# Kernel optimization log

Measured on AMD Instinct MI355X. Metric: run time of the kernel, lower is better.

Reference implementation:

```python
import jax, jax.numpy as jnp
import numpy as np

B, L, DIM, H, D = 4, 1024, 1024, 8, 32


def setup_inputs() -> dict:
    key = jax.random.key(0)
    ks = jax.random.split(key, 8)
    s = 0.02
    return dict(
        x=jax.random.normal(ks[0], (B, L, DIM), jnp.float32),
        W_in=jax.random.normal(ks[1], (DIM, DIM), jnp.float32) * s,
        b_in=jnp.zeros((DIM,), jnp.float32),
        W_qkva=jax.random.normal(ks[2], (H * D * 8, DIM), jnp.float32) * s,
        b_qkva=jnp.zeros((H * D * 8,), jnp.float32),
        W_y=jax.random.normal(ks[3], (DIM, H * D * 2), jnp.float32) * s,
        b_y=jnp.zeros((DIM,), jnp.float32),
        W_out=jax.random.normal(ks[4], (DIM, DIM), jnp.float32) * s,
        b_out=jnp.zeros((DIM,), jnp.float32),
        h0_re=jax.random.normal(ks[5], (H, D, D), jnp.float32),
        h0_im=jax.random.normal(ks[6], (H, D, D), jnp.float32),
    )


def reference(x, W_in, b_in, W_qkva, b_qkva, W_y, b_y, W_out, b_out, h0_re, h0_im):
    b, Ls, dim = x.shape
    Hh, Dd = h0_re.shape[0], h0_re.shape[1]
    u = jax.nn.silu(x @ W_in.T + b_in)
    qkva = (u @ W_qkva.T + b_qkva).reshape(b, Ls, Hh, Dd, 4, 2)
    c = jax.lax.complex(qkva[..., 0], qkva[..., 1])  # [b,L,H,D,4] complex
    q, k, v, a = c[..., 0], c[..., 1], c[..., 2], c[..., 3]
    mag2 = a.real * a.real + a.imag * a.imag
    # unit-modulus rotation scaled by sigmoid(log|a|^2) gate
    a = a * (jax.lax.rsqrt(mag2) * jax.nn.sigmoid(jnp.log(mag2)))
    kv = jnp.einsum('blhd,blhe->blhde', k, v)  # [b,L,H,D,D] complex
    h0 = jax.lax.complex(h0_re, h0_im)[None]  # [1,H,D,D]
    # fold initial state into step 0: h_0 = a_0 * h_init + kv_0
    kv = kv.at[:, 0].add(a[:, 0, ..., None] * h0)
    a_e = a[..., None]  # [b,L,H,D,1], broadcasts over state col dim

    def comb(c1, c2):
        a1, x1 = c1
        a2, x2 = c2
        return (a1 * a2, a2 * x1 + x2)

    # linear recurrence h_l = a_l * h_{l-1} + kv_l (equiv. to the FFT/cumsum
    # triangular-product matrix in the original module)
    _, h = jax.lax.associative_scan(comb, (a_e, kv), axis=1)
    y = jnp.einsum('blhd,blhde->blhe', q, h)  # [b,L,H,D] complex
    y2 = jnp.stack([y.real, y.imag], axis=-1).reshape(b, Ls, Hh * Dd * 2)
    y2 = jax.nn.silu(y2 @ W_y.T + b_y)
    return y2 @ W_out.T + b_out
```

## Files before the change

### kernel.cpp

```cpp
#include <hip/hip_runtime.h>

#define B_ 4
#define L_ 1024
#define DIM_ 1024
#define H_ 8
#define D_ 32
#define LSEG 16
#define NSEG (L_/LSEG)

typedef __bf16 bf16_t;
typedef __bf16 bf16x8 __attribute__((ext_vector_type(8)));
typedef float f32x4 __attribute__((ext_vector_type(4)));

__device__ __forceinline__ void gload_lds16(const bf16_t* g, bf16_t* l) {
  __builtin_amdgcn_global_load_lds((const __attribute__((address_space(1))) void*)g,
                                   (__attribute__((address_space(3))) void*)l, 16, 0, 0);
}
__device__ __forceinline__ void gload_lds16f(const float* g, float* l) {
  __builtin_amdgcn_global_load_lds((const __attribute__((address_space(1))) void*)g,
                                   (__attribute__((address_space(3))) void*)l, 16, 0, 0);
}

__global__ __launch_bounds__(256) void cvt_all(const float* __restrict__ x,
                                               const float* __restrict__ w1,
                                               const float* __restrict__ w2,
                                               const float* __restrict__ w3,
                                               const float* __restrict__ w4,
                                               bf16_t* __restrict__ ox,
                                               bf16_t* __restrict__ o1,
                                               bf16_t* __restrict__ o2,
                                               bf16_t* __restrict__ o3,
                                               bf16_t* __restrict__ o4) {
  int g = blockIdx.x;
  const float* in; bf16_t* out; int i;
  if      (g < 4096) { in = x;  out = ox; i = g * 256 + threadIdx.x; }
  else if (g < 5120) { in = w1; out = o1; i = (g - 4096) * 256 + threadIdx.x; }
  else if (g < 7168) { in = w2; out = o2; i = (g - 5120) * 256 + threadIdx.x; }
  else if (g < 7680) { in = w3; out = o3; i = (g - 7168) * 256 + threadIdx.x; }
  else               { in = w4; out = o4; i = (g - 7680) * 256 + threadIdx.x; }
  float4 v = ((const float4*)in)[i];
  union { bf16_t b[4]; unsigned long long q; } pk;
  pk.b[0] = (bf16_t)v.x; pk.b[1] = (bf16_t)v.y;
  pk.b[2] = (bf16_t)v.z; pk.b[3] = (bf16_t)v.w;
  ((unsigned long long*)out)[i] = pk.q;
}

template<int BN, int ACT, int OUTBF, int GATE>
__global__ __launch_bounds__(256) void gemm_nt(const bf16_t* __restrict__ A,
                                               const bf16_t* __restrict__ Bm,
                                               const float* __restrict__ bias,
                                               void* __restrict__ Cout,
                                               int M, int N, int K) {
  constexpr int NI = BN / 32;
  constexpr int ISS_B = BN / 32;
  __shared__ __align__(16) bf16_t As[128 * 64];
  __shared__ __align__(16) bf16_t Bs[BN * 64];
  const int t = threadIdx.x;
  const int wid = t >> 6, lane = t & 63;
  const int wr = wid >> 1, wc = wid & 1;
  const int lr = lane & 15, lq = lane >> 4;
  const int bm = blockIdx.x, bn = blockIdx.y;
  const int rA = wid * 32 + (lane >> 3);
  const int rB = wid * (BN / 4) + (lane >> 3);
  const int c8 = (((lane & 7) ^ ((lane >> 3) & 7))) * 8;
  const bf16_t* Ag = A + (size_t)(bm * 128 + rA) * K + c8;
  const bf16_t* Bg = Bm + (size_t)(bn * BN + rB) * K + c8;
  bf16_t* AsW = As + (wid * 32) * 64;
  bf16_t* BsW = Bs + (wid * (BN / 4)) * 64;
  f32x4 acc[4][NI] = {};
  for (int k0 = 0; k0 < K; k0 += 64) {
#pragma unroll
    for (int j = 0; j < 4; ++j)
      gload_lds16(Ag + (size_t)j * 8 * K, AsW + j * 8 * 64);
#pragma unroll
    for (int j = 0; j < ISS_B; ++j)
      gload_lds16(Bg + (size_t)j * 8 * K, BsW + j * 8 * 64);
    Ag += 64; Bg += 64;
    __syncthreads();
#pragma unroll
    for (int ks = 0; ks < 2; ++ks) {
      const int sg = ks * 4 + lq;
      const int sl = (sg ^ (lr & 7)) * 8;
      bf16x8 af[4], bfv[NI];
#pragma unroll
      for (int mi = 0; mi < 4; ++mi)
        af[mi] = *(const bf16x8*)&As[(wr * 64 + mi * 16 + lr) * 64 + sl];
#pragma unroll
      for (int ni = 0; ni < NI; ++ni)
        bfv[ni] = *(const bf16x8*)&Bs[(wc * (BN/2) + ni * 16 + lr) * 64 + sl];
#pragma unroll
      for (int mi = 0; mi < 4; ++mi)
#pragma unroll
        for (int ni = 0; ni < NI; ++ni)
          acc[mi][ni] = __builtin_amdgcn_mfma_f32_16x16x32_bf16(af[mi], bfv[ni], acc[mi][ni], 0, 0, 0);
    }
    __syncthreads();
  }
#pragma unroll
  for (int mi = 0; mi < 4; ++mi) {
#pragma unroll
    for (int ni = 0; ni < NI; ++ni) {
      int colg = bn * BN + wc * (BN/2) + ni * 16 + lr;
      float bb = bias[colg];
#pragma unroll
      for (int r = 0; r < 4; ++r) {
        int rowg = bm * 128 + wr * 64 + mi * 16 + lq * 4 + r;
        float v = acc[mi][ni][r] + bb;
        if (ACT == 1) v = v / (1.0f + __expf(-v));
        if (GATE) {
          float wv = __shfl_xor(v, 1);
          if ((colg & 7) >= 6) {
            float m2 = v * v + wv * wv;
            v *= sqrtf(m2) / (1.0f + m2);
          }
        }
        if (OUTBF) ((bf16_t*)Cout)[(size_t)rowg * N + colg] = (bf16_t)v;
        else       ((float*)Cout)[(size_t)rowg * N + colg] = v;
      }
    }
  }
}

template<int ACT, int OUTBF>
__global__ __launch_bounds__(256) void gemm_nt64(const bf16_t* __restrict__ A,
                                                 const bf16_t* __restrict__ Bm,
                                                 const float* __restrict__ bias,
                                                 void* __restrict__ Cout,
                                                 int M, int N, int K) {
  __shared__ __align__(16) bf16_t As[128 * 128];
  __shared__ __align__(16) bf16_t Bs[64 * 128];
  const int t = threadIdx.x;
  const int wid = t >> 6, lane = t & 63;
  const int wr = wid >> 1, wc = wid & 1;
  const int lr = lane & 15, lq = lane >> 4;
  const int bm = blockIdx.x, bn = blockIdx.y;
  const int crow = wid * 4 + (lane >> 4);
  const int c8 = ((lane & 15) ^ crow) * 8;
  const bf16_t* Ag = A + (size_t)(bm * 128 + crow) * K + c8;
  const bf16_t* Bg = Bm + (size_t)(bn * 64 + crow) * K + c8;
  bf16_t* AsW = As + (wid * 4) * 128;
  bf16_t* BsW = Bs + (wid * 4) * 128;
  f32x4 acc[4][2] = {};
  for (int k0 = 0; k0 < K; k0 += 128) {
#pragma unroll
    for (int j = 0; j < 8; ++j)
      gload_lds16(Ag + (size_t)j * 16 * K, AsW + j * 16 * 128);
#pragma unroll
    for (int j = 0; j < 4; ++j)
      gload_lds16(Bg + (size_t)j * 16 * K, BsW + j * 16 * 128);
    Ag += 128; Bg += 128;
    __syncthreads();
#pragma unroll
    for (int ks = 0; ks < 4; ++ks) {
      const int sg = ks * 4 + lq;
      const int sl = (sg ^ lr) * 8;
      bf16x8 af[4], bfv[2];
#pragma unroll
      for (int mi = 0; mi < 4; ++mi)
        af[mi] = *(const bf16x8*)&As[(wr * 64 + mi * 16 + lr) * 128 + sl];
#pragma unroll
      for (int ni = 0; ni < 2; ++ni)
        bfv[ni] = *(const bf16x8*)&Bs[(wc * 32 + ni * 16 + lr) * 128 + sl];
#pragma unroll
      for (int mi = 0; mi < 4; ++mi)
#pragma unroll
        for (int ni = 0; ni < 2; ++ni)
          acc[mi][ni] = __builtin_amdgcn_mfma_f32_16x16x32_bf16(af[mi], bfv[ni], acc[mi][ni], 0, 0, 0);
    }
    __syncthreads();
  }
#pragma unroll
  for (int mi = 0; mi < 4; ++mi) {
#pragma unroll
    for (int ni = 0; ni < 2; ++ni) {
      int colg = bn * 64 + wc * 32 + ni * 16 + lr;
      float bb = bias[colg];
#pragma unroll
      for (int r = 0; r < 4; ++r) {
        int rowg = bm * 128 + wr * 64 + mi * 16 + lq * 4 + r;
        float v = acc[mi][ni][r] + bb;
        if (ACT == 1) v = v / (1.0f + __expf(-v));
        if (OUTBF) ((bf16_t*)Cout)[(size_t)rowg * N + colg] = (bf16_t)v;
        else       ((float*)Cout)[(size_t)rowg * N + colg] = v;
      }
    }
  }
}

__global__ __launch_bounds__(256) void scan_seg(const float* __restrict__ qkva,
                                                float* __restrict__ y_loc,
                                                float* __restrict__ qP,
                                                float* __restrict__ Aseg,
                                                float* __restrict__ Hfin) {
  __shared__ __align__(16) float Q[LSEG * 256];
  const int t = threadIdx.x;
  const int seg = blockIdx.x;
  const int s = seg & (NSEG - 1);
  const int bh = seg >> 6;
  const int h = bh & (H_ - 1), b = bh >> 3;
  const int wid = t >> 6, lane = t & 63;
  const int dg = lane & 7, eh = lane >> 3;
  const int e = wid * 8 + eh;
  const float* gb = qkva + ((size_t)(b * L_ + s * LSEG) * H_ + h) * 256;
#pragma unroll
  for (int j = 0; j < 4; ++j) {
    const int l = wid * 4 + j;
    gload_lds16f(gb + (size_t)l * (H_ * 256) + lane * 4, Q + l * 256);
  }
  __syncthreads();
  float hr[4] = {}, hi[4] = {};
  float Pr[4] = {1,1,1,1}, Pi[4] = {0,0,0,0};
  size_t row = ((size_t)(b * L_ + s * LSEG) * H_ + h) * D_;
  for (int l = 0; l < LSEG; ++l) {
    const float* R = Q + l * 256;
    float2 vv = *(const float2*)(R + e * 8 + 4);
    float ytr = 0.f, yti = 0.f;
    float2 qpv[4];
#pragma unroll
    for (int j = 0; j < 4; ++j) {
      const int d = dg + 8 * j;
      float4 qk = *(const float4*)(R + d * 8);
      float2 aa = *(const float2*)(R + d * 8 + 6);
      float nPr = aa.x * Pr[j] - aa.y * Pi[j];
      float nPi = aa.x * Pi[j] + aa.y * Pr[j];
      Pr[j] = nPr; Pi[j] = nPi;
      qpv[j].x = qk.x * nPr - qk.y * nPi;
      qpv[j].y = qk.x * nPi + qk.y * nPr;
      float kvr = qk.z * vv.x - qk.w * vv.y;
      float kvi = qk.z * vv.y + qk.w * vv.x;
      float nhr = aa.x * hr[j] - aa.y * hi[j] + kvr;
      float nhi = aa.x * hi[j] + aa.y * hr[j] + kvi;
      hr[j] = nhr; hi[j] = nhi;
      ytr += qk.x * nhr - qk.y * nhi;
      yti += qk.x * nhi + qk.y * nhr;
    }
    ytr += __shfl_down(ytr, 4); yti += __shfl_down(yti, 4);
    ytr += __shfl_down(ytr, 2); yti += __shfl_down(yti, 2);
    ytr += __shfl_down(ytr, 1); yti += __shfl_down(yti, 1);
    if (dg == 0)
      *(float2*)(y_loc + (row + e) * 2) = make_float2(ytr, yti);
    if (t < 8) {
#pragma unroll
      for (int j = 0; j < 4; ++j)
        *(float2*)(qP + (row + dg + 8 * j) * 2) = qpv[j];
    }
    row += H_ * D_;
  }
  const size_t segb = (size_t)seg * D_;
  if (t < 8) {
#pragma unroll
    for (int j = 0; j < 4; ++j)
      *(float2*)(Aseg + (segb + dg + 8 * j) * 2) = make_float2(Pr[j], Pi[j]);
  }
#pragma unroll
  for (int j = 0; j < 4; ++j)
    *(float2*)(Hfin + ((segb + dg + 8 * j) * D_ + e) * 2) = make_float2(hr[j], hi[j]);
}

__global__ __launch_bounds__(128) void seg_combine(const float* __restrict__ h0re,
                                                   const float* __restrict__ h0im,
                                                   const float* __restrict__ Aseg,
                                                   const float* __restrict__ Hfin,
                                                   float* __restrict__ Hc) {
  const int bh = blockIdx.x >> 3;
  const int eg = blockIdx.x & 7;
  const int h = bh & (H_ - 1);
  const int t = threadIdx.x;
  const int d = t >> 2;
  const int e = eg * 4 + (t & 3);
  float cr = h0re[((size_t)h * D_ + d) * D_ + e];
  float ci = h0im[((size_t)h * D_ + d) * D_ + e];
  const size_t idx0  = ((size_t)bh * NSEG * D_ + d) * D_ + e;
  const size_t aidx0 = (size_t)bh * NSEG * D_ + d;
  float2 Ab[8], Fb[8];
#pragma unroll
  for (int p = 0; p < 8; ++p) {
    Ab[p] = *(const float2*)(Aseg + (aidx0 + (size_t)p * D_) * 2);
    Fb[p] = *(const float2*)(Hfin + (idx0 + (size_t)p * D_ * D_) * 2);
  }
  for (int so = 0; so < NSEG; so += 8) {
#pragma unroll
    for (int p = 0; p < 8; ++p) {
      const int s = so + p;
      float2 A0 = Ab[p], F0 = Fb[p];
      if (so + 8 < NSEG) {
        Ab[p] = *(const float2*)(Aseg + (aidx0 + (size_t)(s + 8) * D_) * 2);
        Fb[p] = *(const float2*)(Hfin + (idx0 + (size_t)(s + 8) * D_ * D_) * 2);
      }
      *(float2*)(Hc + (idx0 + (size_t)s * D_ * D_) * 2) = make_float2(cr, ci);
      float nr = A0.x * cr - A0.y * ci + F0.x;
      float ni = A0.x * ci + A0.y * cr + F0.y;
      cr = nr; ci = ni;
    }
  }
}

__global__ __launch_bounds__(256) void y_correct(const float* __restrict__ y_loc,
                                                 const float* __restrict__ qP,
                                                 const float* __restrict__ Hc,
                                                 bf16_t* __restrict__ y2b) {
  __shared__ __align__(16) float Hs[D_ * D_ * 2];
  const int seg = blockIdx.x;
  const int s = seg & (NSEG - 1);
  const int bh = seg >> 6;
  const int h = bh & (H_ - 1), b = bh >> 3;
  const int t = threadIdx.x;
  const float4* src = (const float4*)(Hc + (size_t)seg * (D_ * D_ * 2));
  ((float4*)Hs)[t] = src[t];
  ((float4*)Hs)[t + 256] = src[t + 256];
  __syncthreads();
  const int l = t >> 4;
  const int ep = (t & 15) * 2;
  const int lg = s * LSEG + l;
  const size_t rowc = ((size_t)(b * L_ + lg) * H_ + h) * D_;
  const float* qpr = qP + rowc * 2;
  float4 y0 = *(const float4*)(y_loc + (rowc + ep) * 2);
  float ac_r[2] = {y0.x, y0.z}, ac_i[2] = {y0.y, y0.w};
#pragma unroll 4
  for (int d = 0; d < D_; ++d) {
    float2 p = *(const float2*)(qpr + d * 2);
    float4 hv = *(const float4*)&Hs[(d * D_ + ep) * 2];
    ac_r[0] += p.x * hv.x - p.y * hv.y; ac_i[0] += p.x * hv.y + p.y * hv.x;
    ac_r[1] += p.x * hv.z - p.y * hv.w; ac_i[1] += p.x * hv.w + p.y * hv.z;
  }
  union { bf16_t bv[4]; uint2 q; } pk;
  pk.bv[0] = (bf16_t)ac_r[0]; pk.bv[1] = (bf16_t)ac_i[0];
  pk.bv[2] = (bf16_t)ac_r[1]; pk.bv[3] = (bf16_t)ac_i[1];
  *(uint2*)(y2b + (size_t)(b * L_ + lg) * (H_ * D_ * 2) + (h * D_ + ep) * 2) = pk.q;
}

extern "C" void kernel_launch(void* const* d_in, const int* in_sizes, int n_in,
                              void* d_out, int out_size, void* d_ws, size_t ws_size,
                              hipStream_t stream) {
  const float* x      = (const float*)d_in[0];
  const float* W_in   = (const float*)d_in[1];
  const float* b_in   = (const float*)d_in[2];
  const float* W_qkva = (const float*)d_in[3];
  const float* b_qkva = (const float*)d_in[4];
  const float* W_y    = (const float*)d_in[5];
  const float* b_y    = (const float*)d_in[6];
  const float* W_out  = (const float*)d_in[7];
  const float* b_out  = (const float*)d_in[8];
  const float* h0re   = (const float*)d_in[9];
  const float* h0im   = (const float*)d_in[10];

  char* w = (char*)d_ws;
  const size_t MB = 1ull << 20;
  bf16_t* Wb_in   = (bf16_t*)(w + 0*MB);
  bf16_t* Wb_qkva = (bf16_t*)(w + 2*MB);
  bf16_t* Wb_y    = (bf16_t*)(w + 6*MB);
  bf16_t* Wb_out  = (bf16_t*)(w + 7*MB);
  bf16_t* xb      = (bf16_t*)(w + 9*MB);
  float*  qP      = (float*) (w + 9*MB);
  bf16_t* u       = (bf16_t*)(w + 17*MB);
  float*  y_loc   = (float*) (w + 17*MB);
  float*  qkva    = (float*) (w + 25*MB);
  float*  Hc      = (float*) (w + 25*MB);
  bf16_t* y2b     = (bf16_t*)(w + 41*MB);
  bf16_t* z       = (bf16_t*)(w + 45*MB);
  float*  Aseg    = (float*) (w + 57*MB);
  float*  Hfin    = (float*) (w + 58*MB);

  cvt_all<<<8704, 256, 0, stream>>>(x, W_in, W_qkva, W_y, W_out,
                                    xb, Wb_in, Wb_qkva, Wb_y, Wb_out);

  gemm_nt64<1,1><<<dim3(32, 16), 256, 0, stream>>>(xb, Wb_in, b_in, u, 4096, 1024, 1024);
  gemm_nt<128,0,0,1><<<dim3(32, 16), 256, 0, stream>>>(u, Wb_qkva, b_qkva, qkva, 4096, 2048, 1024);
  scan_seg   <<<2048, 256, 0, stream>>>(qkva, y_loc, qP, Aseg, Hfin);
  seg_combine<<<256,  128, 0, stream>>>(h0re, h0im, Aseg, Hfin, Hc);
  y_correct  <<<2048, 256, 0, stream>>>(y_loc, qP, Hc, y2b);
  gemm_nt64<1,1><<<dim3(32, 16), 256, 0, stream>>>(y2b, Wb_y, b_y, z, 4096, 1024, 512);
  gemm_nt64<0,0><<<dim3(32, 16), 256, 0, stream>>>(z, Wb_out, b_out, (float*)d_out, 4096, 1024, 1024);
}
```

Baseline: 229.2 us.

## Fuse segmented scan, combine and correction into one cooperative kernel

Replaces the three-kernel chunked scan (local scan, cross-segment combine, y correction) with a single cooperative-groups kernel that uses grid-wide syncs between phases. Segments grow from 16 to 32 steps, and q·P and local y stay in shared memory instead of round-tripping through global buffers. This removes two launches and the y_loc/qP traffic. In exchange it adds grid sync overhead, a serial combine phase run by only 256 blocks, and it depends on all 1024 blocks being co-resident, with a fallback to the old path otherwise.

```diff
diff --git a/kernel.cpp b/kernel.cpp
--- a/kernel.cpp
+++ b/kernel.cpp
@@ -1,4 +1,5 @@
 #include <hip/hip_runtime.h>
+#include <hip/hip_cooperative_groups.h>
 
 #define B_ 4
 #define L_ 1024
@@ -7,6 +8,8 @@
 #define D_ 32
 #define LSEG 16
 #define NSEG (L_/LSEG)
+#define LSEG2 32
+#define NSEG2 (L_/LSEG2)
 
 typedef __bf16 bf16_t;
 typedef __bf16 bf16x8 __attribute__((ext_vector_type(8)));
@@ -184,6 +187,159 @@
         else       ((float*)Cout)[(size_t)rowg * N + colg] = v;
       }
     }
+  }
+}
+
+__global__ __launch_bounds__(256, 4) void scan_fused(
+    const float* qkva,
+    const float* __restrict__ h0re,
+    const float* __restrict__ h0im,
+    float* __restrict__ Aseg,
+    float* __restrict__ Hfin,
+    float* Hc,
+    bf16_t* y2b) {
+  __shared__ __align__(16) float S[LSEG2 * 256];
+  const int t = threadIdx.x;
+  const int seg = blockIdx.x;
+  const int s = seg & (NSEG2 - 1);
+  const int bh = seg >> 5;
+  const int h = bh & (H_ - 1), b = bh >> 3;
+  const int wid = t >> 6, lane = t & 63;
+  const int dg = lane & 7, eh = lane >> 3;
+  const int e = wid * 8 + eh;
+
+  const float* gb = qkva + ((size_t)(b * L_ + s * LSEG2) * H_ + h) * 256;
+#pragma unroll
+  for (int j = 0; j < 8; ++j) {
+    const int l = wid * 8 + j;
+    gload_lds16f(gb + (size_t)l * (H_ * 256) + lane * 4, S + l * 256);
+  }
+  __syncthreads();
+  float hr[4] = {}, hi[4] = {};
+  float Pr[4] = {1,1,1,1}, Pi[4] = {0,0,0,0};
+  for (int l = 0; l < LSEG2; ++l) {
+    const float* R = S + l * 256;
+    float2 vv = *(const float2*)(R + e * 8 + 4);
+    float ytr = 0.f, yti = 0.f;
+    float2 qpv[4];
+#pragma unroll
+    for (int j = 0; j < 4; ++j) {
+      const int d = dg + 8 * j;
+      float4 qk = *(const float4*)(R + d * 8);
+      float2 aa = *(const float2*)(R + d * 8 + 6);
+      float nPr = aa.x * Pr[j] - aa.y * Pi[j];
+      float nPi = aa.x * Pi[j] + aa.y * Pr[j];
+      Pr[j] = nPr; Pi[j] = nPi;
+      qpv[j].x = qk.x * nPr - qk.y * nPi;
+      qpv[j].y = qk.x * nPi + qk.y * nPr;
+      float kvr = qk.z * vv.x - qk.w * vv.y;
+      float kvi = qk.z * vv.y + qk.w * vv.x;
+      float nhr = aa.x * hr[j] - aa.y * hi[j] + kvr;
+      float nhi = aa.x * hi[j] + aa.y * hr[j] + kvi;
+      hr[j] = nhr; hi[j] = nhi;
+      ytr += qk.x * nhr - qk.y * nhi;
+      yti += qk.x * nhi + qk.y * nhr;
+    }
+    ytr += __shfl_down(ytr, 4); yti += __shfl_down(yti, 4);
+    ytr += __shfl_down(ytr, 2); yti += __shfl_down(yti, 2);
+    ytr += __shfl_down(ytr, 1); yti += __shfl_down(yti, 1);
+    __syncthreads();
+    if (t < 8) {
+#pragma unroll
+      for (int j = 0; j < 4; ++j) {
+        const int d = dg + 8 * j;
+        *(float2*)(S + l * 256 + ((d + l * 4) & 31) * 2) = qpv[j];
+      }
+    }
+    if (dg == 0)
+      *(float2*)(S + l * 256 + 64 + ((e + l * 4) & 31) * 2) = make_float2(ytr, yti);
+  }
+  const size_t segb = (size_t)seg * D_;
+  if (t < 8) {
+#pragma unroll
+    for (int j = 0; j < 4; ++j)
+      *(float2*)(Aseg + (segb + dg + 8 * j) * 2) = make_float2(Pr[j], Pi[j]);
+  }
+#pragma unroll
+  for (int j = 0; j < 4; ++j)
+    *(float2*)(Hfin + ((segb + dg + 8 * j) * D_ + e) * 2) = make_float2(hr[j], hi[j]);
+
+  cooperative_groups::this_grid().sync();
+
+  if (seg < 256 && t < 128) {
+    const int bh2 = seg >> 3;
+    const int eg = seg & 7;
+    const int h2 = bh2 & (H_ - 1);
+    const int d2 = t >> 2;
+    const int e2 = eg * 4 + (t & 3);
+    float cr = h0re[((size_t)h2 * D_ + d2) * D_ + e2];
+    float ci = h0im[((size_t)h2 * D_ + d2) * D_ + e2];
+    const size_t idx0  = ((size_t)bh2 * NSEG2 * D_ + d2) * D_ + e2;
+    const size_t aidx0 = (size_t)bh2 * NSEG2 * D_ + d2;
+    float2 Ab[8], Fb[8];
+#pragma unroll
+    for (int p = 0; p < 8; ++p) {
+      Ab[p] = *(const float2*)(Aseg + (aidx0 + (size_t)p * D_) * 2);
+      Fb[p] = *(const float2*)(Hfin + (idx0 + (size_t)p * D_ * D_) * 2);
+    }
+    for (int so = 0; so < NSEG2; so += 8) {
+#pragma unroll
+      for (int p = 0; p < 8; ++p) {
+        const int s2 = so + p;
+        float2 A0 = Ab[p], F0 = Fb[p];
+        if (so + 8 < NSEG2) {
+          Ab[p] = *(const float2*)(Aseg + (aidx0 + (size_t)(s2 + 8) * D_) * 2);
+          Fb[p] = *(const float2*)(Hfin + (idx0 + (size_t)(s2 + 8) * D_ * D_) * 2);
+        }
+        *(float2*)(Hc + (idx0 + (size_t)s2 * D_ * D_) * 2) = make_float2(cr, ci);
+        float nr = A0.x * cr - A0.y * ci + F0.x;
+        float ni = A0.x * ci + A0.y * cr + F0.y;
+        cr = nr; ci = ni;
+      }
+    }
+  }
+
+  cooperative_groups::this_grid().sync();
+
+  {
+    const float4* src = (const float4*)(Hc + (size_t)seg * (D_ * D_ * 2));
+#pragma unroll
+    for (int k = 0; k < 2; ++k) {
+      float4 v4 = src[k * 256 + t];
+      int F = (k * 256 + t) * 4;
+      int rw = F >> 6, j = F & 63;
+      *(float4*)(S + rw * 256 + 128 + j) = v4;
+    }
+  }
+  __syncthreads();
+  {
+    const int l = t >> 3;
+    const int tg = t & 7;
+    const int e0 = tg * 4;
+    float acr[4], aci[4];
+#pragma unroll
+    for (int i = 0; i < 4; ++i) {
+      float2 y0 = *(const float2*)(S + l * 256 + 64 + ((e0 + i + l * 4) & 31) * 2);
+      acr[i] = y0.x; aci[i] = y0.y;
+    }
+#pragma unroll 4
+    for (int d = 0; d < D_; ++d) {
+      float2 p = *(const float2*)(S + l * 256 + ((d + l * 4) & 31) * 2);
+      float4 h0v = *(const float4*)(S + d * 256 + 128 + e0 * 2);
+      float4 h1v = *(const float4*)(S + d * 256 + 128 + e0 * 2 + 4);
+      acr[0] += p.x * h0v.x - p.y * h0v.y; aci[0] += p.x * h0v.y + p.y * h0v.x;
+      acr[1] += p.x * h0v.z - p.y * h0v.w; aci[1] += p.x * h0v.w + p.y * h0v.z;
+      acr[2] += p.x * h1v.x - p.y * h1v.y; aci[2] += p.x * h1v.y + p.y * h1v.x;
+      acr[3] += p.x * h1v.z - p.y * h1v.w; aci[3] += p.x * h1v.w + p.y * h1v.z;
+    }
+    const int lg = s * LSEG2 + l;
+    union { bf16_t bv[8]; uint4 q; } pk;
+#pragma unroll
+    for (int i = 0; i < 4; ++i) {
+      pk.bv[2 * i]     = (bf16_t)acr[i];
+      pk.bv[2 * i + 1] = (bf16_t)aci[i];
+    }
+    *(uint4*)(y2b + (size_t)(b * L_ + lg) * (H_ * D_ * 2) + ((size_t)h * D_ + e0) * 2) = pk.q;
   }
 }
 
@@ -361,14 +517,31 @@
   float*  Aseg    = (float*) (w + 57*MB);
   float*  Hfin    = (float*) (w + 58*MB);
 
+  static int coop_ok = -1;
+  if (coop_ok < 0) {
+    int nb = 0;
+    hipError_t err = hipOccupancyMaxActiveBlocksPerMultiprocessor(&nb, scan_fused, 256, 0);
+    coop_ok = (err == hipSuccess && nb >= 4) ? 1 : 0;
+  }
+
   cvt_all<<<8704, 256, 0, stream>>>(x, W_in, W_qkva, W_y, W_out,
                                     xb, Wb_in, Wb_qkva, Wb_y, Wb_out);
 
   gemm_nt64<1,1><<<dim3(32, 16), 256, 0, stream>>>(xb, Wb_in, b_in, u, 4096, 1024, 1024);
   gemm_nt<128,0,0,1><<<dim3(32, 16), 256, 0, stream>>>(u, Wb_qkva, b_qkva, qkva, 4096, 2048, 1024);
-  scan_seg   <<<2048, 256, 0, stream>>>(qkva, y_loc, qP, Aseg, Hfin);
-  seg_combine<<<256,  128, 0, stream>>>(h0re, h0im, Aseg, Hfin, Hc);
-  y_correct  <<<2048, 256, 0, stream>>>(y_loc, qP, Hc, y2b);
+
+  if (coop_ok) {
+    const float* qkva_c = qkva;
+    void* args[] = { (void*)&qkva_c, (void*)&h0re, (void*)&h0im,
+                     (void*)&Aseg, (void*)&Hfin, (void*)&Hc, (void*)&y2b };
+    hipLaunchCooperativeKernel((const void*)scan_fused, dim3(1024), dim3(256),
+                               args, 0, stream);
+  } else {
+    scan_seg   <<<2048, 256, 0, stream>>>(qkva, y_loc, qP, Aseg, Hfin);
+    seg_combine<<<256,  128, 0, stream>>>(h0re, h0im, Aseg, Hfin, Hc);
+    y_correct  <<<2048, 256, 0, stream>>>(y_loc, qP, Hc, y2b);
+  }
+
   gemm_nt64<1,1><<<dim3(32, 16), 256, 0, stream>>>(y2b, Wb_y, b_y, z, 4096, 1024, 512);
   gemm_nt64<0,0><<<dim3(32, 16), 256, 0, stream>>>(z, Wb_out, b_out, (float*)d_out, 4096, 1024, 1024);
 }
```

Measured after the change: 229.9 us. No clear change (+0.3%).

## Double-buffer GEMM LDS tiles with async global-to-LDS prefetch

Applied to the files above, without the earlier changes.

Replaces the single-buffered GEMM kernels with a double-buffered variant that issues the next K-tile's global-to-LDS loads before computing on the current tile. Partial vmcnt waits and raw s_barrier calls replace full __syncthreads. The 128-wide-K gemm_nt64 kernel is dropped in favour of the 64-K double-buffered kernel at BN=64 for the three 1024-wide GEMMs. The aim is to hide global memory latency behind MFMA work, at the cost of doubled LDS use (lower occupancy) and fragile hand-counted vmcnt values.

```diff
diff --git a/kernel.cpp b/kernel.cpp
--- a/kernel.cpp
+++ b/kernel.cpp
@@ -46,15 +46,15 @@
 }
 
 template<int BN, int ACT, int OUTBF, int GATE>
-__global__ __launch_bounds__(256) void gemm_nt(const bf16_t* __restrict__ A,
+__global__ __launch_bounds__(256) void gemm_db(const bf16_t* __restrict__ A,
                                                const bf16_t* __restrict__ Bm,
                                                const float* __restrict__ bias,
                                                void* __restrict__ Cout,
                                                int M, int N, int K) {
   constexpr int NI = BN / 32;
-  constexpr int ISS_B = BN / 32;
-  __shared__ __align__(16) bf16_t As[128 * 64];
-  __shared__ __align__(16) bf16_t Bs[BN * 64];
+  constexpr int JB = BN / 32;
+  __shared__ __align__(16) bf16_t As[2][128 * 64];
+  __shared__ __align__(16) bf16_t Bs[2][BN * 64];
   const int t = threadIdx.x;
   const int wid = t >> 6, lane = t & 63;
   const int wr = wid >> 1, wc = wid & 1;
@@ -65,18 +65,32 @@
   const int c8 = (((lane & 7) ^ ((lane >> 3) & 7))) * 8;
   const bf16_t* Ag = A + (size_t)(bm * 128 + rA) * K + c8;
   const bf16_t* Bg = Bm + (size_t)(bn * BN + rB) * K + c8;
-  bf16_t* AsW = As + (wid * 32) * 64;
-  bf16_t* BsW = Bs + (wid * (BN / 4)) * 64;
   f32x4 acc[4][NI] = {};
-  for (int k0 = 0; k0 < K; k0 += 64) {
+
+  auto stage = [&](int bufi, int koff) {
+    bf16_t* AsW = &As[bufi][(wid * 32) * 64];
+    bf16_t* BsW = &Bs[bufi][(wid * (BN / 4)) * 64];
 #pragma unroll
     for (int j = 0; j < 4; ++j)
-      gload_lds16(Ag + (size_t)j * 8 * K, AsW + j * 8 * 64);
-#pragma unroll
-    for (int j = 0; j < ISS_B; ++j)
-      gload_lds16(Bg + (size_t)j * 8 * K, BsW + j * 8 * 64);
-    Ag += 64; Bg += 64;
-    __syncthreads();
+      gload_lds16(Ag + (size_t)koff + (size_t)j * 8 * K, AsW + j * 8 * 64);
+#pragma unroll
+    for (int j = 0; j < JB; ++j)
+      gload_lds16(Bg + (size_t)koff + (size_t)j * 8 * K, BsW + j * 8 * 64);
+  };
+
+  const int NT = K >> 6;
+  stage(0, 0);
+  for (int tt = 0; tt < NT; ++tt) {
+    const int cur = tt & 1;
+    if (tt + 1 < NT) {
+      stage(cur ^ 1, (tt + 1) * 64);
+      if (BN == 128) asm volatile("s_waitcnt vmcnt(8)" ::: "memory");
+      else           asm volatile("s_waitcnt vmcnt(6)" ::: "memory");
+    } else {
+      asm volatile("s_waitcnt vmcnt(0)" ::: "memory");
+    }
+    __builtin_amdgcn_s_barrier();
+    __builtin_amdgcn_sched_barrier(0);
 #pragma unroll
     for (int ks = 0; ks < 2; ++ks) {
       const int sg = ks * 4 + lq;
@@ -84,23 +98,24 @@
       bf16x8 af[4], bfv[NI];
 #pragma unroll
       for (int mi = 0; mi < 4; ++mi)
-        af[mi] = *(const bf16x8*)&As[(wr * 64 + mi * 16 + lr) * 64 + sl];
+        af[mi] = *(const bf16x8*)&As[cur][(wr * 64 + mi * 16 + lr) * 64 + sl];
 #pragma unroll
       for (int ni = 0; ni < NI; ++ni)
-        bfv[ni] = *(const bf16x8*)&Bs[(wc * (BN/2) + ni * 16 + lr) * 64 + sl];
+        bfv[ni] = *(const bf16x8*)&Bs[cur][(wc * (BN / 2) + ni * 16 + lr) * 64 + sl];
 #pragma unroll
       for (int mi = 0; mi < 4; ++mi)
 #pragma unroll
         for (int ni = 0; ni < NI; ++ni)
           acc[mi][ni] = __builtin_amdgcn_mfma_f32_16x16x32_bf16(af[mi], bfv[ni], acc[mi][ni], 0, 0, 0);
     }
-    __syncthreads();
+    __builtin_amdgcn_sched_barrier(0);
+    __builtin_amdgcn_s_barrier();
   }
 #pragma unroll
   for (int mi = 0; mi < 4; ++mi) {
 #pragma unroll
     for (int ni = 0; ni < NI; ++ni) {
-      int colg = bn * BN + wc * (BN/2) + ni * 16 + lr;
+      int colg = bn * BN + wc * (BN / 2) + ni * 16 + lr;
       float bb = bias[colg];
 #pragma unroll
       for (int r = 0; r < 4; ++r) {
@@ -114,72 +129,6 @@
             v *= sqrtf(m2) / (1.0f + m2);
           }
         }
-        if (OUTBF) ((bf16_t*)Cout)[(size_t)rowg * N + colg] = (bf16_t)v;
-        else       ((float*)Cout)[(size_t)rowg * N + colg] = v;
-      }
-    }
-  }
-}
-
-template<int ACT, int OUTBF>
-__global__ __launch_bounds__(256) void gemm_nt64(const bf16_t* __restrict__ A,
-                                                 const bf16_t* __restrict__ Bm,
-                                                 const float* __restrict__ bias,
-                                                 void* __restrict__ Cout,
-                                                 int M, int N, int K) {
-  __shared__ __align__(16) bf16_t As[128 * 128];
-  __shared__ __align__(16) bf16_t Bs[64 * 128];
-  const int t = threadIdx.x;
-  const int wid = t >> 6, lane = t & 63;
-  const int wr = wid >> 1, wc = wid & 1;
-  const int lr = lane & 15, lq = lane >> 4;
-  const int bm = blockIdx.x, bn = blockIdx.y;
-  const int crow = wid * 4 + (lane >> 4);
-  const int c8 = ((lane & 15) ^ crow) * 8;
-  const bf16_t* Ag = A + (size_t)(bm * 128 + crow) * K + c8;
-  const bf16_t* Bg = Bm + (size_t)(bn * 64 + crow) * K + c8;
-  bf16_t* AsW = As + (wid * 4) * 128;
-  bf16_t* BsW = Bs + (wid * 4) * 128;
-  f32x4 acc[4][2] = {};
-  for (int k0 = 0; k0 < K; k0 += 128) {
-#pragma unroll
-    for (int j = 0; j < 8; ++j)
-      gload_lds16(Ag + (size_t)j * 16 * K, AsW + j * 16 * 128);
-#pragma unroll
-    for (int j = 0; j < 4; ++j)
-      gload_lds16(Bg + (size_t)j * 16 * K, BsW + j * 16 * 128);
-    Ag += 128; Bg += 128;
-    __syncthreads();
-#pragma unroll
-    for (int ks = 0; ks < 4; ++ks) {
-      const int sg = ks * 4 + lq;
-      const int sl = (sg ^ lr) * 8;
-      bf16x8 af[4], bfv[2];
-#pragma unroll
-      for (int mi = 0; mi < 4; ++mi)
-        af[mi] = *(const bf16x8*)&As[(wr * 64 + mi * 16 + lr) * 128 + sl];
-#pragma unroll
-      for (int ni = 0; ni < 2; ++ni)
-        bfv[ni] = *(const bf16x8*)&Bs[(wc * 32 + ni * 16 + lr) * 128 + sl];
-#pragma unroll
-      for (int mi = 0; mi < 4; ++mi)
-#pragma unroll
-        for (int ni = 0; ni < 2; ++ni)
-          acc[mi][ni] = __builtin_amdgcn_mfma_f32_16x16x32_bf16(af[mi], bfv[ni], acc[mi][ni], 0, 0, 0);
-    }
-    __syncthreads();
-  }
-#pragma unroll
-  for (int mi = 0; mi < 4; ++mi) {
-#pragma unroll
-    for (int ni = 0; ni < 2; ++ni) {
-      int colg = bn * 64 + wc * 32 + ni * 16 + lr;
-      float bb = bias[colg];
-#pragma unroll
-      for (int r = 0; r < 4; ++r) {
-        int rowg = bm * 128 + wr * 64 + mi * 16 + lq * 4 + r;
-        float v = acc[mi][ni][r] + bb;
-        if (ACT == 1) v = v / (1.0f + __expf(-v));
         if (OUTBF) ((bf16_t*)Cout)[(size_t)rowg * N + colg] = (bf16_t)v;
         else       ((float*)Cout)[(size_t)rowg * N + colg] = v;
       }
@@ -364,11 +313,11 @@
   cvt_all<<<8704, 256, 0, stream>>>(x, W_in, W_qkva, W_y, W_out,
                                     xb, Wb_in, Wb_qkva, Wb_y, Wb_out);
 
-  gemm_nt64<1,1><<<dim3(32, 16), 256, 0, stream>>>(xb, Wb_in, b_in, u, 4096, 1024, 1024);
-  gemm_nt<128,0,0,1><<<dim3(32, 16), 256, 0, stream>>>(u, Wb_qkva, b_qkva, qkva, 4096, 2048, 1024);
+  gemm_db<64,1,1,0><<<dim3(32, 16), 256, 0, stream>>>(xb, Wb_in, b_in, u, 4096, 1024, 1024);
+  gemm_db<128,0,0,1><<<dim3(32, 16), 256, 0, stream>>>(u, Wb_qkva, b_qkva, qkva, 4096, 2048, 1024);
   scan_seg   <<<2048, 256, 0, stream>>>(qkva, y_loc, qP, Aseg, Hfin);
   seg_combine<<<256,  128, 0, stream>>>(h0re, h0im, Aseg, Hfin, Hc);
   y_correct  <<<2048, 256, 0, stream>>>(y_loc, qP, Hc, y2b);
-  gemm_nt64<1,1><<<dim3(32, 16), 256, 0, stream>>>(y2b, Wb_y, b_y, z, 4096, 1024, 512);
-  gemm_nt64<0,0><<<dim3(32, 16), 256, 0, stream>>>(z, Wb_out, b_out, (float*)d_out, 4096, 1024, 1024);
-}
+  gemm_db<64,1,1,0><<<dim3(32, 16), 256, 0, stream>>>(y2b, Wb_y, b_y, z, 4096, 1024, 512);
+  gemm_db<64,0,0,0><<<dim3(32, 16), 256, 0, stream>>>(z, Wb_out, b_out, (float*)d_out, 4096, 1024, 1024);
+}
```

Measured after the change: 232.8 us. Within noise of the previous version (+1.6%).

## Fuse x fp32-to-bf16 conversion into first GEMM and remap blocks across XCDs

Applied to the files above, without the earlier changes.

Drops the separate conversion of the 16MB fp32 input x to bf16. The first GEMM now reads fp32 x directly, converts it in registers and writes bf16 into LDS, which removes a full write and re-read of the activation through global memory. The weight-only conversion kernel stays. Separately, all GEMMs remap block IDs so consecutive tiles land on the same XCD, aiming for better L2 reuse. The fused A load goes through registers instead of direct-to-LDS loads and reads twice the bytes per tile, which may expose more load latency.

```diff
diff --git a/kernel.cpp b/kernel.cpp
--- a/kernel.cpp
+++ b/kernel.cpp
@@ -21,23 +21,28 @@
                                    (__attribute__((address_space(3))) void*)l, 16, 0, 0);
 }
 
-__global__ __launch_bounds__(256) void cvt_all(const float* __restrict__ x,
-                                               const float* __restrict__ w1,
-                                               const float* __restrict__ w2,
-                                               const float* __restrict__ w3,
-                                               const float* __restrict__ w4,
-                                               bf16_t* __restrict__ ox,
-                                               bf16_t* __restrict__ o1,
-                                               bf16_t* __restrict__ o2,
-                                               bf16_t* __restrict__ o3,
-                                               bf16_t* __restrict__ o4) {
+__device__ __forceinline__ void xcd_remap(int& bm, int& bn) {
+  const int id = blockIdx.x + 32 * blockIdx.y;
+  const int nwg = 32 * gridDim.y;
+  const int wk = (id & 7) * (nwg >> 3) + (id >> 3);
+  bm = wk & 31;
+  bn = wk >> 5;
+}
+
+__global__ __launch_bounds__(256) void cvt_w(const float* __restrict__ w1,
+                                             const float* __restrict__ w2,
+                                             const float* __restrict__ w3,
+                                             const float* __restrict__ w4,
+                                             bf16_t* __restrict__ o1,
+                                             bf16_t* __restrict__ o2,
+                                             bf16_t* __restrict__ o3,
+                                             bf16_t* __restrict__ o4) {
   int g = blockIdx.x;
   const float* in; bf16_t* out; int i;
-  if      (g < 4096) { in = x;  out = ox; i = g * 256 + threadIdx.x; }
-  else if (g < 5120) { in = w1; out = o1; i = (g - 4096) * 256 + threadIdx.x; }
-  else if (g < 7168) { in = w2; out = o2; i = (g - 5120) * 256 + threadIdx.x; }
-  else if (g < 7680) { in = w3; out = o3; i = (g - 7168) * 256 + threadIdx.x; }
-  else               { in = w4; out = o4; i = (g - 7680) * 256 + threadIdx.x; }
+  if      (g < 1024) { in = w1; out = o1; i = g * 256 + threadIdx.x; }
+  else if (g < 3072) { in = w2; out = o2; i = (g - 1024) * 256 + threadIdx.x; }
+  else if (g < 3584) { in = w3; out = o3; i = (g - 3072) * 256 + threadIdx.x; }
+  else               { in = w4; out = o4; i = (g - 3584) * 256 + threadIdx.x; }
   float4 v = ((const float4*)in)[i];
   union { bf16_t b[4]; unsigned long long q; } pk;
   pk.b[0] = (bf16_t)v.x; pk.b[1] = (bf16_t)v.y;
@@ -59,7 +64,7 @@
   const int wid = t >> 6, lane = t & 63;
   const int wr = wid >> 1, wc = wid & 1;
   const int lr = lane & 15, lq = lane >> 4;
-  const int bm = blockIdx.x, bn = blockIdx.y;
+  int bm, bn; xcd_remap(bm, bn);
   const int rA = wid * 32 + (lane >> 3);
   const int rB = wid * (BN / 4) + (lane >> 3);
   const int c8 = (((lane & 7) ^ ((lane >> 3) & 7))) * 8;
@@ -133,7 +138,7 @@
   const int wid = t >> 6, lane = t & 63;
   const int wr = wid >> 1, wc = wid & 1;
   const int lr = lane & 15, lq = lane >> 4;
-  const int bm = blockIdx.x, bn = blockIdx.y;
+  int bm, bn; xcd_remap(bm, bn);
   const int crow = wid * 4 + (lane >> 4);
   const int c8 = ((lane & 15) ^ crow) * 8;
   const bf16_t* Ag = A + (size_t)(bm * 128 + crow) * K + c8;
@@ -148,6 +153,88 @@
 #pragma unroll
     for (int j = 0; j < 4; ++j)
       gload_lds16(Bg + (size_t)j * 16 * K, BsW + j * 16 * 128);
+    Ag += 128; Bg += 128;
+    __syncthreads();
+#pragma unroll
+    for (int ks = 0; ks < 4; ++ks) {
+      const int sg = ks * 4 + lq;
+      const int sl = (sg ^ lr) * 8;
+      bf16x8 af[4], bfv[2];
+#pragma unroll
+      for (int mi = 0; mi < 4; ++mi)
+        af[mi] = *(const bf16x8*)&As[(wr * 64 + mi * 16 + lr) * 128 + sl];
+#pragma unroll
+      for (int ni = 0; ni < 2; ++ni)
+        bfv[ni] = *(const bf16x8*)&Bs[(wc * 32 + ni * 16 + lr) * 128 + sl];
+#pragma unroll
+      for (int mi = 0; mi < 4; ++mi)
+#pragma unroll
+        for (int ni = 0; ni < 2; ++ni)
+          acc[mi][ni] = __builtin_amdgcn_mfma_f32_16x16x32_bf16(af[mi], bfv[ni], acc[mi][ni], 0, 0, 0);
+    }
+    __syncthreads();
+  }
+#pragma unroll
+  for (int mi = 0; mi < 4; ++mi) {
+#pragma unroll
+    for (int ni = 0; ni < 2; ++ni) {
+      int colg = bn * 64 + wc * 32 + ni * 16 + lr;
+      float bb = bias[colg];
+#pragma unroll
+      for (int r = 0; r < 4; ++r) {
+        int rowg = bm * 128 + wr * 64 + mi * 16 + lq * 4 + r;
+        float v = acc[mi][ni][r] + bb;
+        if (ACT == 1) v = v / (1.0f + __expf(-v));
+        if (OUTBF) ((bf16_t*)Cout)[(size_t)rowg * N + colg] = (bf16_t)v;
+        else       ((float*)Cout)[(size_t)rowg * N + colg] = v;
+      }
+    }
+  }
+}
+
+template<int ACT, int OUTBF>
+__global__ __launch_bounds__(256) void gemm_a32(const float* __restrict__ A32,
+                                                const bf16_t* __restrict__ Bm,
+                                                const float* __restrict__ bias,
+                                                void* __restrict__ Cout,
+                                                int M, int N, int K) {
+  __shared__ __align__(16) bf16_t As[128 * 128];
+  __shared__ __align__(16) bf16_t Bs[64 * 128];
+  const int t = threadIdx.x;
+  const int wid = t >> 6, lane = t & 63;
+  const int wr = wid >> 1, wc = wid & 1;
+  const int lr = lane & 15, lq = lane >> 4;
+  int bm, bn; xcd_remap(bm, bn);
+  const int crow = wid * 4 + (lane >> 4);
+  const int c8 = ((lane & 15) ^ crow) * 8;
+  const float*  Ag = A32 + (size_t)(bm * 128 + crow) * K + c8;
+  const bf16_t* Bg = Bm + (size_t)(bn * 64 + crow) * K + c8;
+  bf16_t* BsW = Bs + (wid * 4) * 128;
+  bf16_t* AsW = As + (size_t)crow * 128 + (lane & 15) * 8;
+  f32x4 acc[4][2] = {};
+  for (int k0 = 0; k0 < K; k0 += 128) {
+#pragma unroll
+    for (int j = 0; j < 4; ++j)
+      gload_lds16(Bg + (size_t)j * 16 * K, BsW + j * 16 * 128);
+#pragma unroll
+    for (int jj = 0; jj < 2; ++jj) {
+      float4 v0[4], v1[4];
+#pragma unroll
+      for (int j = 0; j < 4; ++j) {
+        const float* p = Ag + (size_t)(jj * 4 + j) * 16 * K;
+        v0[j] = *(const float4*)p;
+        v1[j] = *(const float4*)(p + 4);
+      }
+#pragma unroll
+      for (int j = 0; j < 4; ++j) {
+        union { bf16x8 v; bf16_t b[8]; } pk;
+        pk.b[0] = (bf16_t)v0[j].x; pk.b[1] = (bf16_t)v0[j].y;
+        pk.b[2] = (bf16_t)v0[j].z; pk.b[3] = (bf16_t)v0[j].w;
+        pk.b[4] = (bf16_t)v1[j].x; pk.b[5] = (bf16_t)v1[j].y;
+        pk.b[6] = (bf16_t)v1[j].z; pk.b[7] = (bf16_t)v1[j].w;
+        *(bf16x8*)(AsW + (size_t)(jj * 4 + j) * 16 * 128) = pk.v;
+      }
+    }
     Ag += 128; Bg += 128;
     __syncthreads();
 #pragma unroll
@@ -350,7 +437,6 @@
   bf16_t* Wb_qkva = (bf16_t*)(w + 2*MB);
   bf16_t* Wb_y    = (bf16_t*)(w + 6*MB);
   bf16_t* Wb_out  = (bf16_t*)(w + 7*MB);
-  bf16_t* xb      = (bf16_t*)(w + 9*MB);
   float*  qP      = (float*) (w + 9*MB);
   bf16_t* u       = (bf16_t*)(w + 17*MB);
   float*  y_loc   = (float*) (w + 17*MB);
@@ -361,10 +447,10 @@
   float*  Aseg    = (float*) (w + 57*MB);
   float*  Hfin    = (float*) (w + 58*MB);
 
-  cvt_all<<<8704, 256, 0, stream>>>(x, W_in, W_qkva, W_y, W_out,
-                                    xb, Wb_in, Wb_qkva, Wb_y, Wb_out);
-
-  gemm_nt64<1,1><<<dim3(32, 16), 256, 0, stream>>>(xb, Wb_in, b_in, u, 4096, 1024, 1024);
+  cvt_w<<<4608, 256, 0, stream>>>(W_in, W_qkva, W_y, W_out,
+                                  Wb_in, Wb_qkva, Wb_y, Wb_out);
+
+  gemm_a32<1,1><<<dim3(32, 16), 256, 0, stream>>>(x, Wb_in, b_in, u, 4096, 1024, 1024);
   gemm_nt<128,0,0,1><<<dim3(32, 16), 256, 0, stream>>>(u, Wb_qkva, b_qkva, qkva, 4096, 2048, 1024);
   scan_seg   <<<2048, 256, 0, stream>>>(qkva, y_loc, qP, Aseg, Hfin);
   seg_combine<<<256,  128, 0, stream>>>(h0re, h0im, Aseg, Hfin, Hc);
```

Result: slower. 262.1 us (+14.4%).
